# Performance work log

Hardware: AMD Instinct MI355X
Metric: run time of the kernel (lower is better)

## Reference

```python
import jax, jax.numpy as jnp
import numpy as np

DT = 0.05        # Euler step size
S_EULER = 2      # Euler steps between consecutive events, and after the last one (prop_to_end)


def setup_inputs() -> dict:
    key = jax.random.key(0)
    B, H, D, K, E = 512, 512, 128, 64, 256
    ks = jax.random.split(key, 16)

    def w(k, fan_in, fan_out):
        return jax.random.normal(k, (fan_in, fan_out), jnp.float32) / np.float32(np.sqrt(fan_in))

    X = jax.random.normal(ks[0], (K, E, D), jnp.float32)
    M = jax.random.bernoulli(ks[1], 0.5, (K, E, D)).astype(jnp.float32)
    # unique sample indices per event (irregular observation pattern, no scatter collisions)
    batch_idx = jax.vmap(lambda k: jax.random.permutation(k, B)[:E])(jax.random.split(ks[2], K))
    sample_idx = jnp.arange(B)
    b = lambda n: jnp.full((n,), 0.01, jnp.float32)  # torch init: bias filled with 0.01
    return {
        'X': X, 'M': M, 'batch_idx': batch_idx, 'sample_idx': sample_idx,
        'Wi': w(ks[3], D + H, H), 'bi': b(H),
        'Wf': w(ks[4], D + H, H), 'bf': b(H),
        'Wo': w(ks[5], D + H, H), 'bo': b(H),
        'Wc': w(ks[6], D + H, H), 'bc': b(H),
        'W1': w(ks[7], H, H), 'b1': b(H),
        'W2': w(ks[8], H, H), 'b2': b(H),
        'Wp1': w(ks[9], H, H), 'bp1': b(H),
        'Wp2': w(ks[10], H, D), 'bp2': b(D),
    }


def reference(X, M, batch_idx, sample_idx,
              Wi, bi, Wf, bf, Wo, bo, Wc, bc,
              W1, b1, W2, b2, Wp1, bp1, Wp2, bp2):
    B = sample_idx.shape[0]
    H = W1.shape[0]
    h0 = jnp.zeros((B, H), X.dtype)
    c0 = jnp.zeros((B, H), X.dtype)

    def euler(h):  # h <- h + dt * ODEFunc(h)
        return h + DT * (jnp.tanh(h @ W1 + b1) @ W2 + b2)

    def p_model(h):  # Linear -> ReLU -> (Dropout p=0, eval) -> Linear
        return jax.nn.relu(h @ Wp1 + bp1) @ Wp2 + bp2

    def step(carry, xs):
        h, c, loss, tot_m = carry
        Xo, Mo, idx = xs  # [E,D], [E,D], [E]
        for _ in range(S_EULER):
            h = euler(h)
        p = p_model(h)
        loss = loss + jnp.sum(jnp.abs(Xo - p[idx]) * Mo)
        tot_m = tot_m + jnp.sum(Mo)
        inp = jnp.concatenate([Xo, h[idx]], axis=-1)  # [E, D+H]
        ig = jax.nn.sigmoid(inp @ Wi + bi)
        fg = jax.nn.sigmoid(inp @ Wf + bf)
        og = jax.nn.sigmoid(inp @ Wo + bo)
        ct = jnp.tanh(inp @ Wc + bc)
        c_new = fg * c[idx] + ig * ct
        h_new = og * jnp.tanh(c_new)
        return (h.at[idx].set(h_new), c.at[idx].set(c_new), loss, tot_m), None

    init = (h0, c0, jnp.float32(0.0), jnp.float32(0.0))
    (h, c, loss, tot_m), _ = jax.lax.scan(step, init, (X, M, batch_idx))
    for _ in range(S_EULER):  # prop_to_end up to T
        h = euler(h)
    return jnp.stack([loss, loss / tot_m])
```

## Files before the change

kernel.cpp:

```cpp
#include <hip/hip_runtime.h>
#include <hip/hip_fp16.h>
#include <stdint.h>

#define Kn 64
#define En 256
#define Bn 512
#define Hn 512
#define Dn 128
#define NBLK 256
#define NTH  256
#define DT_C 0.05f


typedef _Float16 f16x8 __attribute__((ext_vector_type(8)));
typedef float    f32x4 __attribute__((ext_vector_type(4)));
typedef unsigned long long u64;

__device__ __forceinline__ float sigm(float x){ return 1.0f/(1.0f + __expf(-x)); }

__device__ __forceinline__ u64 ald(const u64* p){
  return __hip_atomic_load(p, __ATOMIC_RELAXED, __HIP_MEMORY_SCOPE_AGENT);
}
__device__ __forceinline__ void ast(u64* p, u64 v){
  __hip_atomic_store(p, v, __ATOMIC_RELAXED, __HIP_MEMORY_SCOPE_AGENT);
}

union HU { __half h[8]; u64 q[2]; };

__global__ void k_init(int* __restrict__ pos, float* __restrict__ acc,
                       int* __restrict__ flg, uint32_t* __restrict__ hf){
  int i = blockIdx.x*blockDim.x + threadIdx.x;
  if (i < Kn*Bn) pos[i] = -1;
  if (i < 2) acc[i] = 0.0f;
  if (i < 32*8*32) flg[i] = 0;
  if (i < Hn*Hn/2) hf[i] = 0;
}

__global__ void k_scatter(const int* __restrict__ bidx, int* __restrict__ pos){
  int i = blockIdx.x*blockDim.x + threadIdx.x;
  if (i < Kn*En){
    int k = i >> 8;
    int e = i & (En-1);
    pos[(k << 9) | bidx[i]] = e;
  }
}

__global__ void k_cvt_frag(const float* __restrict__ src, __half* __restrict__ dst,
                           int KT, int N, int n){
  int i = blockIdx.x*blockDim.x + threadIdx.x;
  if (i >= n) return;
  int C = i / (KT*512);
  int r = i % (KT*512);
  int T = r >> 9;
  int q = r & 511;
  int l = q >> 3, e = q & 7;
  int srow = T*32 + ((l>>4)<<3) + e;
  int scol = C*16 + (l&15);
  dst[i] = __float2half(src[(size_t)srow*N + scol]);
}

__device__ __forceinline__ f32x4 mv16(const __half* Af, const f16x8* Wr, int lane){
  f32x4 a = {0.f,0.f,0.f,0.f};
  #pragma unroll
  for (int kt=0; kt<16; kt++){
    f16x8 av = *(const f16x8*)(Af + kt*512 + lane*8);
    a = __builtin_amdgcn_mfma_f32_16x16x32_f16(av, Wr[kt], a, 0,0,0);
  }
  return a;
}

__global__ __launch_bounds__(NTH, 1) void k_main(
  const float* __restrict__ X, const float* __restrict__ Mm,
  const int* __restrict__ pos, const __half* __restrict__ WF,
  __half* __restrict__ Hf, __half* __restrict__ Tf,
  __half* __restrict__ T2f, __half* __restrict__ Hf2,
  const float* __restrict__ bi_, const float* __restrict__ bf_,
  const float* __restrict__ bo_, const float* __restrict__ bc_,
  const float* __restrict__ b1_, const float* __restrict__ b2_,
  const float* __restrict__ bp1_, const float* __restrict__ bp2_,
  float* __restrict__ acc, int* __restrict__ flg)
{
  const __half* W1F  = WF;
  const __half* W2F  = WF + 262144;
  const __half* Wp1F = WF + 524288;
  const __half* Wp2F = WF + 786432;
  const __half* WgF  = WF + 851968;

  const int t    = threadIdx.x;
  const int bid  = blockIdx.x;
  const int s    = bid & 7;
  const int g    = bid >> 3;
  const int w    = t >> 6;
  const int lane = t & 63;
  int* flgbase = flg + g*8*32;

  __shared__ __align__(16) __half Afrag[16*512];
  __shared__ __align__(16) __half Bfrag[16*512];
  __shared__ __align__(16) __half Xfrag[4*512];
  __shared__ __align__(16) float  outb[20*256];
  __shared__ float redbuf[8];

  const int row = t >> 4;
  const int q4  = t & 15;
  const int sc  = s*64 + q4*4;
  float Hreg[4] = {0,0,0,0};
  float Creg[4] = {0,0,0,0};
  float vb1[4], vb2[4], vbp1[4], vbi[4], vbf[4], vbo[4], vbc[4];
  #pragma unroll
  for (int i=0;i<4;i++){
    vb1[i]=b1_[sc+i]; vb2[i]=b2_[sc+i]; vbp1[i]=bp1_[sc+i];
    vbi[i]=bi_[sc+i]; vbf[i]=bf_[sc+i]; vbo[i]=bo_[sc+i]; vbc[i]=bc_[sc+i];
  }
  const float vbp2 = bp2_[s*16 + q4];

  f16x8 W1r[16], W2r[16], Wp1r[16];
  {
    const size_t cb = (size_t)(s*4 + w)*16*512 + (size_t)lane*8;
    #pragma unroll
    for (int kt=0; kt<16; kt++){
      W1r[kt]  = *(const f16x8*)(W1F  + cb + kt*512);
      W2r[kt]  = *(const f16x8*)(W2F  + cb + kt*512);
      Wp1r[kt] = *(const f16x8*)(Wp1F + cb + kt*512);
    }
  }

  float loss_loc = 0.f, m_loc = 0.f;
  int rnd = 0;
  const int grow = g*16 + row;

#define POLL() do{                                                         \
    if (t < 8){                                                            \
      while (__hip_atomic_load(flgbase + t*32, __ATOMIC_RELAXED,           \
                               __HIP_MEMORY_SCOPE_AGENT) < rnd)            \
        __builtin_amdgcn_s_sleep(1);                                       \
    }                                                                      \
    __syncthreads();                                                       \
  }while(0)

#define PUBLISH() do{                                                      \
    asm volatile("s_waitcnt vmcnt(0)" ::: "memory");                       \
    __syncthreads();                                                       \
    rnd++;                                                                 \
    if (t == 0)                                                            \
      __hip_atomic_store(flgbase + s*32, rnd, __ATOMIC_RELAXED,            \
                         __HIP_MEMORY_SCOPE_AGENT);                        \
  }while(0)

#define STAGE(DST, SRCPTR) do{                                             \
    const int ar = t & 15, ch = t >> 4;                                    \
    const u64* sp = (const u64*)((SRCPTR) + ((size_t)(g*16+ar))*512 + ch*32); \
    u64 v[8];                                                              \
    _Pragma("unroll") for (int i=0;i<8;i++) v[i] = ald(sp+i);              \
    _Pragma("unroll")                                                      \
    for (int kg=0;kg<4;kg++){                                              \
      u64* d = (u64*)((DST) + ch*512 + (ar + 16*kg)*8);                    \
      d[0] = v[2*kg]; d[1] = v[2*kg+1];                                    \
    }                                                                      \
  }while(0)

  for (int k=0; k<Kn; k++){
    const int epos = pos[(k<<9) + grow];

    POLL();
    if (k > 0) STAGE(Bfrag, T2f);
    {
      const int ar = t & 15, ch = t >> 4;
      const __half* hsrc = Hf;
      if (k > 0 && pos[((k-1)<<9) + g*16 + ar] >= 0) hsrc = Hf2;
      const u64* sp = (const u64*)(hsrc + ((size_t)(g*16+ar))*512 + ch*32);
      u64 v[8];
      #pragma unroll
      for (int i=0;i<8;i++) v[i] = ald(sp+i);
      #pragma unroll
      for (int kg=0;kg<4;kg++){
        u64* d = (u64*)(Afrag + ch*512 + (ar + 16*kg)*8);
        d[0] = v[2*kg]; d[1] = v[2*kg+1];
      }
    }
    __syncthreads();
    {
      f32x4 a4 = mv16(Afrag, W1r, lane);
      float* o = outb + w*256 + ((lane>>4)*4)*16 + (lane&15);
      o[0]=a4[0]; o[16]=a4[1]; o[32]=a4[2]; o[48]=a4[3];
    }
    if (k > 0){
      const __half* wb = Wp2F + (size_t)s*16*512;
      f32x4 a4 = {0,0,0,0};
      #pragma unroll
      for (int kt2=0; kt2<4; kt2++){
        const int kt = w*4 + kt2;
        f16x8 a = *(const f16x8*)(Bfrag + kt*512 + lane*8);
        f16x8 b = *(const f16x8*)(wb + kt*512 + lane*8);
        a4 = __builtin_amdgcn_mfma_f32_16x16x32_f16(a, b, a4, 0,0,0);
      }
      float* o = outb + (16+w)*256 + ((lane>>4)*4)*16 + (lane&15);
      o[0]=a4[0]; o[16]=a4[1]; o[32]=a4[2]; o[48]=a4[3];
    }
    __syncthreads();
    {
      const float* o = outb + (q4>>2)*256 + row*16 + (q4&3)*4;
      HU u;
      u.h[0]=__float2half(tanhf(o[0]+vb1[0])); u.h[1]=__float2half(tanhf(o[1]+vb1[1]));
      u.h[2]=__float2half(tanhf(o[2]+vb1[2])); u.h[3]=__float2half(tanhf(o[3]+vb1[3]));
      ast((u64*)(Tf + (size_t)grow*512 + sc), u.q[0]);
    }
    PUBLISH();
    if (k > 0){
      const int ep = pos[((k-1)<<9) + g*16 + row];
      if (ep >= 0){
        float p = outb[16*256 + row*16+q4] + outb[17*256 + row*16+q4]
                + outb[18*256 + row*16+q4] + outb[19*256 + row*16+q4] + vbp2;
        const size_t xo = ((size_t)((k-1)*En+ep))*Dn + s*16 + q4;
        float mo = Mm[xo];
        loss_loc += fabsf(X[xo] - p)*mo;
        m_loc    += mo;
      }
    }

    POLL();
    STAGE(Afrag, Tf);
    __syncthreads();
    {
      f32x4 a4 = mv16(Afrag, W2r, lane);
      float* o = outb + w*256 + ((lane>>4)*4)*16 + (lane&15);
      o[0]=a4[0]; o[16]=a4[1]; o[32]=a4[2]; o[48]=a4[3];
    }
    __syncthreads();
    {
      const float* o = outb + (q4>>2)*256 + row*16 + (q4&3)*4;
      HU u;
      Hreg[0] += DT_C*(o[0]+vb2[0]); Hreg[1] += DT_C*(o[1]+vb2[1]);
      Hreg[2] += DT_C*(o[2]+vb2[2]); Hreg[3] += DT_C*(o[3]+vb2[3]);
      u.h[0]=__float2half(Hreg[0]); u.h[1]=__float2half(Hreg[1]);
      u.h[2]=__float2half(Hreg[2]); u.h[3]=__float2half(Hreg[3]);
      ast((u64*)(Hf + (size_t)grow*512 + sc), u.q[0]);
    }
    PUBLISH();

    POLL();
    STAGE(Afrag, Hf);
    __syncthreads();
    {
      f32x4 a4 = mv16(Afrag, W1r, lane);
      float* o = outb + w*256 + ((lane>>4)*4)*16 + (lane&15);
      o[0]=a4[0]; o[16]=a4[1]; o[32]=a4[2]; o[48]=a4[3];
    }
    __syncthreads();
    {
      const float* o = outb + (q4>>2)*256 + row*16 + (q4&3)*4;
      HU u;
      u.h[0]=__float2half(tanhf(o[0]+vb1[0])); u.h[1]=__float2half(tanhf(o[1]+vb1[1]));
      u.h[2]=__float2half(tanhf(o[2]+vb1[2])); u.h[3]=__float2half(tanhf(o[3]+vb1[3]));
      ast((u64*)(Tf + (size_t)grow*512 + sc), u.q[0]);
    }
    PUBLISH();

    POLL();
    STAGE(Afrag, Tf);
    __syncthreads();
    {
      f32x4 a4 = mv16(Afrag, W2r, lane);
      float* o = outb + w*256 + ((lane>>4)*4)*16 + (lane&15);
      o[0]=a4[0]; o[16]=a4[1]; o[32]=a4[2]; o[48]=a4[3];
    }
    __syncthreads();
    {
      const float* o = outb + (q4>>2)*256 + row*16 + (q4&3)*4;
      HU u;
      Hreg[0] += DT_C*(o[0]+vb2[0]); Hreg[1] += DT_C*(o[1]+vb2[1]);
      Hreg[2] += DT_C*(o[2]+vb2[2]); Hreg[3] += DT_C*(o[3]+vb2[3]);
      u.h[0]=__float2half(Hreg[0]); u.h[1]=__float2half(Hreg[1]);
      u.h[2]=__float2half(Hreg[2]); u.h[3]=__float2half(Hreg[3]);
      ast((u64*)(Hf + (size_t)grow*512 + sc), u.q[0]);
    }
    PUBLISH();

    POLL();
    STAGE(Afrag, Hf);
    if (t < 64){
      const int ar = t & 15, ch = t >> 4;
      const int e = pos[(k<<9) + g*16 + ar];
      float xv[32];
      if (e >= 0){
        const float4* xp = (const float4*)(X + ((size_t)(k*En+e))*Dn + ch*32);
        #pragma unroll
        for (int i=0;i<8;i++){
          float4 f = xp[i];
          xv[4*i]=f.x; xv[4*i+1]=f.y; xv[4*i+2]=f.z; xv[4*i+3]=f.w;
        }
      } else {
        #pragma unroll
        for (int i=0;i<32;i++) xv[i]=0.f;
      }
      #pragma unroll
      for (int kg=0;kg<4;kg++){
        HU u;
        #pragma unroll
        for (int e8=0;e8<8;e8++) u.h[e8] = __float2half(xv[kg*8+e8]);
        u64* d = (u64*)(Xfrag + ch*512 + (ar + 16*kg)*8);
        d[0] = u.q[0]; d[1] = u.q[1];
      }
    }
    __syncthreads();
    {
      f32x4 a4 = mv16(Afrag, Wp1r, lane);
      float* o = outb + (16+w)*256 + ((lane>>4)*4)*16 + (lane&15);
      o[0]=a4[0]; o[16]=a4[1]; o[32]=a4[2]; o[48]=a4[3];
    }
    #pragma unroll 1
    for (int i=0;i<4;i++){
      const int Cg = w*32 + s*4 + i;
      const __half* wb = WgF + (size_t)Cg*20*512;
      f32x4 a4 = {0,0,0,0};
      #pragma unroll 4
      for (int kt=0; kt<4; kt++){
        f16x8 a = *(const f16x8*)(Xfrag + kt*512 + lane*8);
        f16x8 b = *(const f16x8*)(wb + kt*512 + lane*8);
        a4 = __builtin_amdgcn_mfma_f32_16x16x32_f16(a, b, a4, 0,0,0);
      }
      #pragma unroll 4
      for (int kt=4; kt<20; kt++){
        f16x8 a = *(const f16x8*)(Afrag + (kt-4)*512 + lane*8);
        f16x8 b = *(const f16x8*)(wb + kt*512 + lane*8);
        a4 = __builtin_amdgcn_mfma_f32_16x16x32_f16(a, b, a4, 0,0,0);
      }
      float* o = outb + (w*4+i)*256 + ((lane>>4)*4)*16 + (lane&15);
      o[0]=a4[0]; o[16]=a4[1]; o[32]=a4[2]; o[48]=a4[3];
    }
    __syncthreads();
    {
      const float* o = outb + (16+(q4>>2))*256 + row*16 + (q4&3)*4;
      HU u;
      u.h[0]=__float2half(fmaxf(o[0]+vbp1[0],0.f));
      u.h[1]=__float2half(fmaxf(o[1]+vbp1[1],0.f));
      u.h[2]=__float2half(fmaxf(o[2]+vbp1[2],0.f));
      u.h[3]=__float2half(fmaxf(o[3]+vbp1[3],0.f));
      ast((u64*)(T2f + (size_t)grow*512 + sc), u.q[0]);
    }
    if (epos >= 0){
      const int sub = q4 >> 2, off = row*16 + (q4&3)*4;
      const float4 pi = *(const float4*)(outb + (0*4+sub)*256 + off);
      const float4 pf = *(const float4*)(outb + (1*4+sub)*256 + off);
      const float4 po = *(const float4*)(outb + (2*4+sub)*256 + off);
      const float4 pc = *(const float4*)(outb + (3*4+sub)*256 + off);
      HU hu;
      const float gi[4]={pi.x,pi.y,pi.z,pi.w}, gf[4]={pf.x,pf.y,pf.z,pf.w};
      const float go[4]={po.x,po.y,po.z,po.w}, gc[4]={pc.x,pc.y,pc.z,pc.w};
      #pragma unroll
      for (int i=0;i<4;i++){
        float ig = sigm(gi[i] + vbi[i]);
        float fg = sigm(gf[i] + vbf[i]);
        float og = sigm(go[i] + vbo[i]);
        float ct = tanhf(gc[i] + vbc[i]);
        Creg[i] = fg*Creg[i] + ig*ct;
        Hreg[i] = og*tanhf(Creg[i]);
        hu.h[i] = __float2half(Hreg[i]);
      }
      ast((u64*)(Hf2 + (size_t)grow*512 + sc), hu.q[0]);
    }
    PUBLISH();
  }

  POLL();
  STAGE(Bfrag, T2f);
  __syncthreads();
  {
    const __half* wb = Wp2F + (size_t)s*16*512;
    f32x4 a4 = {0,0,0,0};
    #pragma unroll
    for (int kt2=0; kt2<4; kt2++){
      const int kt = w*4 + kt2;
      f16x8 a = *(const f16x8*)(Bfrag + kt*512 + lane*8);
      f16x8 b = *(const f16x8*)(wb + kt*512 + lane*8);
      a4 = __builtin_amdgcn_mfma_f32_16x16x32_f16(a, b, a4, 0,0,0);
    }
    float* o = outb + (16+w)*256 + ((lane>>4)*4)*16 + (lane&15);
    o[0]=a4[0]; o[16]=a4[1]; o[32]=a4[2]; o[48]=a4[3];
  }
  __syncthreads();
  {
    const int ep = pos[((Kn-1)<<9) + g*16 + row];
    if (ep >= 0){
      float p = outb[16*256 + row*16+q4] + outb[17*256 + row*16+q4]
              + outb[18*256 + row*16+q4] + outb[19*256 + row*16+q4] + vbp2;
      const size_t xo = ((size_t)((Kn-1)*En+ep))*Dn + s*16 + q4;
      float mo = Mm[xo];
      loss_loc += fabsf(X[xo] - p)*mo;
      m_loc    += mo;
    }
  }

  #pragma unroll
  for (int off=32; off>0; off>>=1){
    loss_loc += __shfl_down(loss_loc, off);
    m_loc    += __shfl_down(m_loc, off);
  }
  if (lane == 0){ redbuf[w] = loss_loc; redbuf[4+w] = m_loc; }
  __syncthreads();
  if (t == 0){
    atomicAdd(acc+0, redbuf[0]+redbuf[1]+redbuf[2]+redbuf[3]);
    atomicAdd(acc+1, redbuf[4]+redbuf[5]+redbuf[6]+redbuf[7]);
  }
#undef POLL
#undef PUBLISH
#undef STAGE
}

__global__ void k_fin(const float* __restrict__ acc, float* __restrict__ out){
  if (threadIdx.x == 0){
    out[0] = acc[0];
    out[1] = acc[0]/acc[1];
  }
}

extern "C" void kernel_launch(void* const* d_in, const int* in_sizes, int n_in,
                              void* d_out, int out_size, void* d_ws, size_t ws_size,
                              hipStream_t stream)
{
  const float* X   = (const float*)d_in[0];
  const float* Mm  = (const float*)d_in[1];
  const int*  bidx = (const int*)d_in[2];
  const float* Wi  = (const float*)d_in[4];
  const float* bi  = (const float*)d_in[5];
  const float* Wf  = (const float*)d_in[6];
  const float* bff = (const float*)d_in[7];
  const float* Wo  = (const float*)d_in[8];
  const float* bo  = (const float*)d_in[9];
  const float* Wc  = (const float*)d_in[10];
  const float* bc  = (const float*)d_in[11];
  const float* W1  = (const float*)d_in[12];
  const float* b1  = (const float*)d_in[13];
  const float* W2  = (const float*)d_in[14];
  const float* b2  = (const float*)d_in[15];
  const float* Wp1 = (const float*)d_in[16];
  const float* bp1 = (const float*)d_in[17];
  const float* Wp2 = (const float*)d_in[18];
  const float* bp2 = (const float*)d_in[19];

  char* ws = (char*)d_ws;
  int*    pos = (int*)ws;
  float*  acc = (float*)(ws + 131072);
  int*    flg = (int*)(ws + 196608);
  __half* Hf  = (__half*)(ws + 1048576);
  __half* Tf  = (__half*)(ws + 1572864);
  __half* T2f = (__half*)(ws + 2097152);
  __half* Hf2 = (__half*)(ws + 2621440);
  __half* WF  = (__half*)(ws + 4194304);

  k_init   <<<512, 256, 0, stream>>>(pos, acc, flg, (uint32_t*)Hf);
  k_scatter<<<(Kn*En + 255)/256, 256, 0, stream>>>(bidx, pos);

  k_cvt_frag<<<(262144+255)/256, 256, 0, stream>>>(W1,  WF,          16, 512, 262144);
  k_cvt_frag<<<(262144+255)/256, 256, 0, stream>>>(W2,  WF + 262144, 16, 512, 262144);
  k_cvt_frag<<<(262144+255)/256, 256, 0, stream>>>(Wp1, WF + 524288, 16, 512, 262144);
  k_cvt_frag<<<(65536 +255)/256, 256, 0, stream>>>(Wp2, WF + 786432, 16, 128, 65536);
  k_cvt_frag<<<(327680+255)/256, 256, 0, stream>>>(Wi,  WF + 851968,            20, 512, 327680);
  k_cvt_frag<<<(327680+255)/256, 256, 0, stream>>>(Wf,  WF + 851968 + 327680,   20, 512, 327680);
  k_cvt_frag<<<(327680+255)/256, 256, 0, stream>>>(Wo,  WF + 851968 + 655360,   20, 512, 327680);
  k_cvt_frag<<<(327680+255)/256, 256, 0, stream>>>(Wc,  WF + 851968 + 983040,   20, 512, 327680);

  k_main<<<NBLK, NTH, 0, stream>>>(X, Mm, pos, WF, Hf, Tf, T2f, Hf2,
                                   bi, bff, bo, bc, b1, b2, bp1, bp2, acc, flg);
  k_fin<<<1, 64, 0, stream>>>(acc, (float*)d_out);
}
```

Baseline: 1.893 ms.

## Halve block count so each block handles two row groups interleaved

Drops the persistent grid from 256 to 128 blocks. Each block now processes two 16-row groups in turn within every phase, keeping separate H/C register state per group and polling or publishing per-group flags. While one group waits on its flags, the other group's work can fill the gap, and fewer blocks share the MI355X's CUs. The cost is twice the serial work per block on the critical path, which may lengthen each phase.

```diff
diff --git a/kernel.cpp b/kernel.cpp
--- a/kernel.cpp
+++ b/kernel.cpp
@@ -7,7 +7,7 @@
 #define Bn 512
 #define Hn 512
 #define Dn 128
-#define NBLK 256
+#define NBLK 128
 #define NTH  256
 #define DT_C 0.05f
 
@@ -89,10 +89,9 @@
   const int t    = threadIdx.x;
   const int bid  = blockIdx.x;
   const int s    = bid & 7;
-  const int g    = bid >> 3;
+  const int qp   = bid >> 3;
   const int w    = t >> 6;
   const int lane = t & 63;
-  int* flgbase = flg + g*8*32;
 
   __shared__ __align__(16) __half Afrag[16*512];
   __shared__ __align__(16) __half Bfrag[16*512];
@@ -103,8 +102,8 @@
   const int row = t >> 4;
   const int q4  = t & 15;
   const int sc  = s*64 + q4*4;
-  float Hreg[4] = {0,0,0,0};
-  float Creg[4] = {0,0,0,0};
+  float Hreg[2][4] = {{0,0,0,0},{0,0,0,0}};
+  float Creg[2][4] = {{0,0,0,0},{0,0,0,0}};
   float vb1[4], vb2[4], vbp1[4], vbi[4], vbf[4], vbo[4], vbc[4];
   #pragma unroll
   for (int i=0;i<4;i++){
@@ -126,29 +125,27 @@
 
   float loss_loc = 0.f, m_loc = 0.f;
   int rnd = 0;
-  const int grow = g*16 + row;
-
-#define POLL() do{                                                         \
+
+#define POLLF(FB, R) do{                                                   \
     if (t < 8){                                                            \
-      while (__hip_atomic_load(flgbase + t*32, __ATOMIC_RELAXED,           \
-                               __HIP_MEMORY_SCOPE_AGENT) < rnd)            \
+      while (__hip_atomic_load((FB) + t*32, __ATOMIC_RELAXED,              \
+                               __HIP_MEMORY_SCOPE_AGENT) < (R))            \
         __builtin_amdgcn_s_sleep(1);                                       \
     }                                                                      \
     __syncthreads();                                                       \
   }while(0)
 
-#define PUBLISH() do{                                                      \
+#define PUBF(FB, R) do{                                                    \
     asm volatile("s_waitcnt vmcnt(0)" ::: "memory");                       \
     __syncthreads();                                                       \
-    rnd++;                                                                 \
     if (t == 0)                                                            \
-      __hip_atomic_store(flgbase + s*32, rnd, __ATOMIC_RELAXED,            \
+      __hip_atomic_store((FB) + s*32, (R), __ATOMIC_RELAXED,               \
                          __HIP_MEMORY_SCOPE_AGENT);                        \
   }while(0)
 
-#define STAGE(DST, SRCPTR) do{                                             \
+#define STAGE(DST, SRCPTR, G) do{                                          \
     const int ar = t & 15, ch = t >> 4;                                    \
-    const u64* sp = (const u64*)((SRCPTR) + ((size_t)(g*16+ar))*512 + ch*32); \
+    const u64* sp = (const u64*)((SRCPTR) + ((size_t)((G)*16+ar))*512 + ch*32); \
     u64 v[8];                                                              \
     _Pragma("unroll") for (int i=0;i<8;i++) v[i] = ald(sp+i);              \
     _Pragma("unroll")                                                      \
@@ -159,31 +156,250 @@
   }while(0)
 
   for (int k=0; k<Kn; k++){
-    const int epos = pos[(k<<9) + grow];
-
-    POLL();
-    if (k > 0) STAGE(Bfrag, T2f);
-    {
-      const int ar = t & 15, ch = t >> 4;
-      const __half* hsrc = Hf;
-      if (k > 0 && pos[((k-1)<<9) + g*16 + ar] >= 0) hsrc = Hf2;
-      const u64* sp = (const u64*)(hsrc + ((size_t)(g*16+ar))*512 + ch*32);
-      u64 v[8];
-      #pragma unroll
-      for (int i=0;i<8;i++) v[i] = ald(sp+i);
-      #pragma unroll
-      for (int kg=0;kg<4;kg++){
-        u64* d = (u64*)(Afrag + ch*512 + (ar + 16*kg)*8);
-        d[0] = v[2*kg]; d[1] = v[2*kg+1];
-      }
-    }
+    #pragma unroll
+    for (int c=0;c<2;c++){
+      const int g = qp*2 + c;
+      int* fb = flg + g*8*32;
+      const int grow = g*16 + row;
+      POLLF(fb, rnd);
+      if (k > 0) STAGE(Bfrag, T2f, g);
+      {
+        const int ar = t & 15, ch = t >> 4;
+        const __half* hsrc = Hf;
+        if (k > 0 && pos[((k-1)<<9) + g*16 + ar] >= 0) hsrc = Hf2;
+        const u64* sp = (const u64*)(hsrc + ((size_t)(g*16+ar))*512 + ch*32);
+        u64 v[8];
+        #pragma unroll
+        for (int i=0;i<8;i++) v[i] = ald(sp+i);
+        #pragma unroll
+        for (int kg=0;kg<4;kg++){
+          u64* d = (u64*)(Afrag + ch*512 + (ar + 16*kg)*8);
+          d[0] = v[2*kg]; d[1] = v[2*kg+1];
+        }
+      }
+      __syncthreads();
+      {
+        f32x4 a4 = mv16(Afrag, W1r, lane);
+        float* o = outb + w*256 + ((lane>>4)*4)*16 + (lane&15);
+        o[0]=a4[0]; o[16]=a4[1]; o[32]=a4[2]; o[48]=a4[3];
+      }
+      if (k > 0){
+        const __half* wb = Wp2F + (size_t)s*16*512;
+        f32x4 a4 = {0,0,0,0};
+        #pragma unroll
+        for (int kt2=0; kt2<4; kt2++){
+          const int kt = w*4 + kt2;
+          f16x8 a = *(const f16x8*)(Bfrag + kt*512 + lane*8);
+          f16x8 b = *(const f16x8*)(wb + kt*512 + lane*8);
+          a4 = __builtin_amdgcn_mfma_f32_16x16x32_f16(a, b, a4, 0,0,0);
+        }
+        float* o = outb + (16+w)*256 + ((lane>>4)*4)*16 + (lane&15);
+        o[0]=a4[0]; o[16]=a4[1]; o[32]=a4[2]; o[48]=a4[3];
+      }
+      __syncthreads();
+      {
+        const float* o = outb + (q4>>2)*256 + row*16 + (q4&3)*4;
+        HU u;
+        u.h[0]=__float2half(tanhf(o[0]+vb1[0])); u.h[1]=__float2half(tanhf(o[1]+vb1[1]));
+        u.h[2]=__float2half(tanhf(o[2]+vb1[2])); u.h[3]=__float2half(tanhf(o[3]+vb1[3]));
+        ast((u64*)(Tf + (size_t)grow*512 + sc), u.q[0]);
+      }
+      PUBF(fb, rnd+1);
+      if (k > 0){
+        const int ep = pos[((k-1)<<9) + g*16 + row];
+        if (ep >= 0){
+          float p = outb[16*256 + row*16+q4] + outb[17*256 + row*16+q4]
+                  + outb[18*256 + row*16+q4] + outb[19*256 + row*16+q4] + vbp2;
+          const size_t xo = ((size_t)((k-1)*En+ep))*Dn + s*16 + q4;
+          float mo = Mm[xo];
+          loss_loc += fabsf(X[xo] - p)*mo;
+          m_loc    += mo;
+        }
+      }
+    }
+    rnd++;
+
+    #pragma unroll
+    for (int c=0;c<2;c++){
+      const int g = qp*2 + c;
+      int* fb = flg + g*8*32;
+      const int grow = g*16 + row;
+      POLLF(fb, rnd);
+      STAGE(Afrag, Tf, g);
+      __syncthreads();
+      {
+        f32x4 a4 = mv16(Afrag, W2r, lane);
+        float* o = outb + w*256 + ((lane>>4)*4)*16 + (lane&15);
+        o[0]=a4[0]; o[16]=a4[1]; o[32]=a4[2]; o[48]=a4[3];
+      }
+      __syncthreads();
+      {
+        const float* o = outb + (q4>>2)*256 + row*16 + (q4&3)*4;
+        HU u;
+        Hreg[c][0] += DT_C*(o[0]+vb2[0]); Hreg[c][1] += DT_C*(o[1]+vb2[1]);
+        Hreg[c][2] += DT_C*(o[2]+vb2[2]); Hreg[c][3] += DT_C*(o[3]+vb2[3]);
+        u.h[0]=__float2half(Hreg[c][0]); u.h[1]=__float2half(Hreg[c][1]);
+        u.h[2]=__float2half(Hreg[c][2]); u.h[3]=__float2half(Hreg[c][3]);
+        ast((u64*)(Hf + (size_t)grow*512 + sc), u.q[0]);
+      }
+      PUBF(fb, rnd+1);
+    }
+    rnd++;
+
+    #pragma unroll
+    for (int c=0;c<2;c++){
+      const int g = qp*2 + c;
+      int* fb = flg + g*8*32;
+      const int grow = g*16 + row;
+      POLLF(fb, rnd);
+      STAGE(Afrag, Hf, g);
+      __syncthreads();
+      {
+        f32x4 a4 = mv16(Afrag, W1r, lane);
+        float* o = outb + w*256 + ((lane>>4)*4)*16 + (lane&15);
+        o[0]=a4[0]; o[16]=a4[1]; o[32]=a4[2]; o[48]=a4[3];
+      }
+      __syncthreads();
+      {
+        const float* o = outb + (q4>>2)*256 + row*16 + (q4&3)*4;
+        HU u;
+        u.h[0]=__float2half(tanhf(o[0]+vb1[0])); u.h[1]=__float2half(tanhf(o[1]+vb1[1]));
+        u.h[2]=__float2half(tanhf(o[2]+vb1[2])); u.h[3]=__float2half(tanhf(o[3]+vb1[3]));
+        ast((u64*)(Tf + (size_t)grow*512 + sc), u.q[0]);
+      }
+      PUBF(fb, rnd+1);
+    }
+    rnd++;
+
+    #pragma unroll
+    for (int c=0;c<2;c++){
+      const int g = qp*2 + c;
+      int* fb = flg + g*8*32;
+      const int grow = g*16 + row;
+      POLLF(fb, rnd);
+      STAGE(Afrag, Tf, g);
+      __syncthreads();
+      {
+        f32x4 a4 = mv16(Afrag, W2r, lane);
+        float* o = outb + w*256 + ((lane>>4)*4)*16 + (lane&15);
+        o[0]=a4[0]; o[16]=a4[1]; o[32]=a4[2]; o[48]=a4[3];
+      }
+      __syncthreads();
+      {
+        const float* o = outb + (q4>>2)*256 + row*16 + (q4&3)*4;
+        HU u;
+        Hreg[c][0] += DT_C*(o[0]+vb2[0]); Hreg[c][1] += DT_C*(o[1]+vb2[1]);
+        Hreg[c][2] += DT_C*(o[2]+vb2[2]); Hreg[c][3] += DT_C*(o[3]+vb2[3]);
+        u.h[0]=__float2half(Hreg[c][0]); u.h[1]=__float2half(Hreg[c][1]);
+        u.h[2]=__float2half(Hreg[c][2]); u.h[3]=__float2half(Hreg[c][3]);
+        ast((u64*)(Hf + (size_t)grow*512 + sc), u.q[0]);
+      }
+      PUBF(fb, rnd+1);
+    }
+    rnd++;
+
+    #pragma unroll
+    for (int c=0;c<2;c++){
+      const int g = qp*2 + c;
+      int* fb = flg + g*8*32;
+      const int grow = g*16 + row;
+      const int epos = pos[(k<<9) + grow];
+      POLLF(fb, rnd);
+      STAGE(Afrag, Hf, g);
+      if (t < 64){
+        const int ar = t & 15, ch = t >> 4;
+        const int e = pos[(k<<9) + g*16 + ar];
+        float xv[32];
+        if (e >= 0){
+          const float4* xp = (const float4*)(X + ((size_t)(k*En+e))*Dn + ch*32);
+          #pragma unroll
+          for (int i=0;i<8;i++){
+            float4 f = xp[i];
+            xv[4*i]=f.x; xv[4*i+1]=f.y; xv[4*i+2]=f.z; xv[4*i+3]=f.w;
+          }
+        } else {
+          #pragma unroll
+          for (int i=0;i<32;i++) xv[i]=0.f;
+        }
+        #pragma unroll
+        for (int kg=0;kg<4;kg++){
+          HU u;
+          #pragma unroll
+          for (int e8=0;e8<8;e8++) u.h[e8] = __float2half(xv[kg*8+e8]);
+          u64* d = (u64*)(Xfrag + ch*512 + (ar + 16*kg)*8);
+          d[0] = u.q[0]; d[1] = u.q[1];
+        }
+      }
+      __syncthreads();
+      {
+        f32x4 a4 = mv16(Afrag, Wp1r, lane);
+        float* o = outb + (16+w)*256 + ((lane>>4)*4)*16 + (lane&15);
+        o[0]=a4[0]; o[16]=a4[1]; o[32]=a4[2]; o[48]=a4[3];
+      }
+      #pragma unroll 1
+      for (int i=0;i<4;i++){
+        const int Cg = w*32 + s*4 + i;
+        const __half* wb = WgF + (size_t)Cg*20*512;
+        f32x4 a4 = {0,0,0,0};
+        #pragma unroll 4
+        for (int kt=0; kt<4; kt++){
+          f16x8 a = *(const f16x8*)(Xfrag + kt*512 + lane*8);
+          f16x8 b = *(const f16x8*)(wb + kt*512 + lane*8);
+          a4 = __builtin_amdgcn_mfma_f32_16x16x32_f16(a, b, a4, 0,0,0);
+        }
+        #pragma unroll 4
+        for (int kt=4; kt<20; kt++){
+          f16x8 a = *(const f16x8*)(Afrag + (kt-4)*512 + lane*8);
+          f16x8 b = *(const f16x8*)(wb + kt*512 + lane*8);
+          a4 = __builtin_amdgcn_mfma_f32_16x16x32_f16(a, b, a4, 0,0,0);
+        }
+        float* o = outb + (w*4+i)*256 + ((lane>>4)*4)*16 + (lane&15);
+        o[0]=a4[0]; o[16]=a4[1]; o[32]=a4[2]; o[48]=a4[3];
+      }
+      __syncthreads();
+      {
+        const float* o = outb + (16+(q4>>2))*256 + row*16 + (q4&3)*4;
+        HU u;
+        u.h[0]=__float2half(fmaxf(o[0]+vbp1[0],0.f));
+        u.h[1]=__float2half(fmaxf(o[1]+vbp1[1],0.f));
+        u.h[2]=__float2half(fmaxf(o[2]+vbp1[2],0.f));
+        u.h[3]=__float2half(fmaxf(o[3]+vbp1[3],0.f));
+        ast((u64*)(T2f + (size_t)grow*512 + sc), u.q[0]);
+      }
+      if (epos >= 0){
+        const int sub = q4 >> 2, off = row*16 + (q4&3)*4;
+        const float4 pi = *(const float4*)(outb + (0*4+sub)*256 + off);
+        const float4 pf = *(const float4*)(outb + (1*4+sub)*256 + off);
+        const float4 po = *(const float4*)(outb + (2*4+sub)*256 + off);
+        const float4 pc = *(const float4*)(outb + (3*4+sub)*256 + off);
+        HU hu;
+        const float gi[4]={pi.x,pi.y,pi.z,pi.w}, gf[4]={pf.x,pf.y,pf.z,pf.w};
+        const float go[4]={po.x,po.y,po.z,po.w}, gc[4]={pc.x,pc.y,pc.z,pc.w};
+        #pragma unroll
+        for (int i=0;i<4;i++){
+          float ig = sigm(gi[i] + vbi[i]);
+          float fg = sigm(gf[i] + vbf[i]);
+          float og = sigm(go[i] + vbo[i]);
+          float ct = tanhf(gc[i] + vbc[i]);
+          Creg[c][i] = fg*Creg[c][i] + ig*ct;
+          Hreg[c][i] = og*tanhf(Creg[c][i]);
+          hu.h[i] = __float2half(Hreg[c][i]);
+        }
+        ast((u64*)(Hf2 + (size_t)grow*512 + sc), hu.q[0]);
+      }
+      PUBF(fb, rnd+1);
+    }
+    rnd++;
+  }
+
+  #pragma unroll
+  for (int c=0;c<2;c++){
+    const int g = qp*2 + c;
+    int* fb = flg + g*8*32;
+    POLLF(fb, rnd);
+    STAGE(Bfrag, T2f, g);
     __syncthreads();
     {
-      f32x4 a4 = mv16(Afrag, W1r, lane);
-      float* o = outb + w*256 + ((lane>>4)*4)*16 + (lane&15);
-      o[0]=a4[0]; o[16]=a4[1]; o[32]=a4[2]; o[48]=a4[3];
-    }
-    if (k > 0){
       const __half* wb = Wp2F + (size_t)s*16*512;
       f32x4 a4 = {0,0,0,0};
       #pragma unroll
@@ -198,196 +414,17 @@
     }
     __syncthreads();
     {
-      const float* o = outb + (q4>>2)*256 + row*16 + (q4&3)*4;
-      HU u;
-      u.h[0]=__float2half(tanhf(o[0]+vb1[0])); u.h[1]=__float2half(tanhf(o[1]+vb1[1]));
-      u.h[2]=__float2half(tanhf(o[2]+vb1[2])); u.h[3]=__float2half(tanhf(o[3]+vb1[3]));
-      ast((u64*)(Tf + (size_t)grow*512 + sc), u.q[0]);
-    }
-    PUBLISH();
-    if (k > 0){
-      const int ep = pos[((k-1)<<9) + g*16 + row];
+      const int ep = pos[((Kn-1)<<9) + g*16 + row];
       if (ep >= 0){
         float p = outb[16*256 + row*16+q4] + outb[17*256 + row*16+q4]
                 + outb[18*256 + row*16+q4] + outb[19*256 + row*16+q4] + vbp2;
-        const size_t xo = ((size_t)((k-1)*En+ep))*Dn + s*16 + q4;
+        const size_t xo = ((size_t)((Kn-1)*En+ep))*Dn + s*16 + q4;
         float mo = Mm[xo];
         loss_loc += fabsf(X[xo] - p)*mo;
         m_loc    += mo;
       }
     }
-
-    POLL();
-    STAGE(Afrag, Tf);
     __syncthreads();
-    {
-      f32x4 a4 = mv16(Afrag, W2r, lane);
-      float* o = outb + w*256 + ((lane>>4)*4)*16 + (lane&15);
-      o[0]=a4[0]; o[16]=a4[1]; o[32]=a4[2]; o[48]=a4[3];
-    }
-    __syncthreads();
-    {
-      const float* o = outb + (q4>>2)*256 + row*16 + (q4&3)*4;
-      HU u;
-      Hreg[0] += DT_C*(o[0]+vb2[0]); Hreg[1] += DT_C*(o[1]+vb2[1]);
-      Hreg[2] += DT_C*(o[2]+vb2[2]); Hreg[3] += DT_C*(o[3]+vb2[3]);
-      u.h[0]=__float2half(Hreg[0]); u.h[1]=__float2half(Hreg[1]);
-      u.h[2]=__float2half(Hreg[2]); u.h[3]=__float2half(Hreg[3]);
-      ast((u64*)(Hf + (size_t)grow*512 + sc), u.q[0]);
-    }
-    PUBLISH();
-
-    POLL();
-    STAGE(Afrag, Hf);
-    __syncthreads();
-    {
-      f32x4 a4 = mv16(Afrag, W1r, lane);
-      float* o = outb + w*256 + ((lane>>4)*4)*16 + (lane&15);
-      o[0]=a4[0]; o[16]=a4[1]; o[32]=a4[2]; o[48]=a4[3];
-    }
-    __syncthreads();
-    {
-      const float* o = outb + (q4>>2)*256 + row*16 + (q4&3)*4;
-      HU u;
-      u.h[0]=__float2half(tanhf(o[0]+vb1[0])); u.h[1]=__float2half(tanhf(o[1]+vb1[1]));
-      u.h[2]=__float2half(tanhf(o[2]+vb1[2])); u.h[3]=__float2half(tanhf(o[3]+vb1[3]));
-      ast((u64*)(Tf + (size_t)grow*512 + sc), u.q[0]);
-    }
-    PUBLISH();
-
-    POLL();
-    STAGE(Afrag, Tf);
-    __syncthreads();
-    {
-      f32x4 a4 = mv16(Afrag, W2r, lane);
-      float* o = outb + w*256 + ((lane>>4)*4)*16 + (lane&15);
-      o[0]=a4[0]; o[16]=a4[1]; o[32]=a4[2]; o[48]=a4[3];
-    }
-    __syncthreads();
-    {
-      const float* o = outb + (q4>>2)*256 + row*16 + (q4&3)*4;
-      HU u;
-      Hreg[0] += DT_C*(o[0]+vb2[0]); Hreg[1] += DT_C*(o[1]+vb2[1]);
-      Hreg[2] += DT_C*(o[2]+vb2[2]); Hreg[3] += DT_C*(o[3]+vb2[3]);
-      u.h[0]=__float2half(Hreg[0]); u.h[1]=__float2half(Hreg[1]);
-      u.h[2]=__float2half(Hreg[2]); u.h[3]=__float2half(Hreg[3]);
-      ast((u64*)(Hf + (size_t)grow*512 + sc), u.q[0]);
-    }
-    PUBLISH();
-
-    POLL();
-    STAGE(Afrag, Hf);
-    if (t < 64){
-      const int ar = t & 15, ch = t >> 4;
-      const int e = pos[(k<<9) + g*16 + ar];
-      float xv[32];
-      if (e >= 0){
-        const float4* xp = (const float4*)(X + ((size_t)(k*En+e))*Dn + ch*32);
-        #pragma unroll
-        for (int i=0;i<8;i++){
-          float4 f = xp[i];
-          xv[4*i]=f.x; xv[4*i+1]=f.y; xv[4*i+2]=f.z; xv[4*i+3]=f.w;
-        }
-      } else {
-        #pragma unroll
-        for (int i=0;i<32;i++) xv[i]=0.f;
-      }
-      #pragma unroll
-      for (int kg=0;kg<4;kg++){
-        HU u;
-        #pragma unroll
-        for (int e8=0;e8<8;e8++) u.h[e8] = __float2half(xv[kg*8+e8]);
-        u64* d = (u64*)(Xfrag + ch*512 + (ar + 16*kg)*8);
-        d[0] = u.q[0]; d[1] = u.q[1];
-      }
-    }
-    __syncthreads();
-    {
-      f32x4 a4 = mv16(Afrag, Wp1r, lane);
-      float* o = outb + (16+w)*256 + ((lane>>4)*4)*16 + (lane&15);
-      o[0]=a4[0]; o[16]=a4[1]; o[32]=a4[2]; o[48]=a4[3];
-    }
-    #pragma unroll 1
-    for (int i=0;i<4;i++){
-      const int Cg = w*32 + s*4 + i;
-      const __half* wb = WgF + (size_t)Cg*20*512;
-      f32x4 a4 = {0,0,0,0};
-      #pragma unroll 4
-      for (int kt=0; kt<4; kt++){
-        f16x8 a = *(const f16x8*)(Xfrag + kt*512 + lane*8);
-        f16x8 b = *(const f16x8*)(wb + kt*512 + lane*8);
-        a4 = __builtin_amdgcn_mfma_f32_16x16x32_f16(a, b, a4, 0,0,0);
-      }
-      #pragma unroll 4
-      for (int kt=4; kt<20; kt++){
-        f16x8 a = *(const f16x8*)(Afrag + (kt-4)*512 + lane*8);
-        f16x8 b = *(const f16x8*)(wb + kt*512 + lane*8);
-        a4 = __builtin_amdgcn_mfma_f32_16x16x32_f16(a, b, a4, 0,0,0);
-      }
-      float* o = outb + (w*4+i)*256 + ((lane>>4)*4)*16 + (lane&15);
-      o[0]=a4[0]; o[16]=a4[1]; o[32]=a4[2]; o[48]=a4[3];
-    }
-    __syncthreads();
-    {
-      const float* o = outb + (16+(q4>>2))*256 + row*16 + (q4&3)*4;
-      HU u;
-      u.h[0]=__float2half(fmaxf(o[0]+vbp1[0],0.f));
-      u.h[1]=__float2half(fmaxf(o[1]+vbp1[1],0.f));
-      u.h[2]=__float2half(fmaxf(o[2]+vbp1[2],0.f));
-      u.h[3]=__float2half(fmaxf(o[3]+vbp1[3],0.f));
-      ast((u64*)(T2f + (size_t)grow*512 + sc), u.q[0]);
-    }
-    if (epos >= 0){
-      const int sub = q4 >> 2, off = row*16 + (q4&3)*4;
-      const float4 pi = *(const float4*)(outb + (0*4+sub)*256 + off);
-      const float4 pf = *(const float4*)(outb + (1*4+sub)*256 + off);
-      const float4 po = *(const float4*)(outb + (2*4+sub)*256 + off);
-      const float4 pc = *(const float4*)(outb + (3*4+sub)*256 + off);
-      HU hu;
-      const float gi[4]={pi.x,pi.y,pi.z,pi.w}, gf[4]={pf.x,pf.y,pf.z,pf.w};
-      const float go[4]={po.x,po.y,po.z,po.w}, gc[4]={pc.x,pc.y,pc.z,pc.w};
-      #pragma unroll
-      for (int i=0;i<4;i++){
-        float ig = sigm(gi[i] + vbi[i]);
-        float fg = sigm(gf[i] + vbf[i]);
-        float og = sigm(go[i] + vbo[i]);
-        float ct = tanhf(gc[i] + vbc[i]);
-        Creg[i] = fg*Creg[i] + ig*ct;
-        Hreg[i] = og*tanhf(Creg[i]);
-        hu.h[i] = __float2half(Hreg[i]);
-      }
-      ast((u64*)(Hf2 + (size_t)grow*512 + sc), hu.q[0]);
-    }
-    PUBLISH();
-  }
-
-  POLL();
-  STAGE(Bfrag, T2f);
-  __syncthreads();
-  {
-    const __half* wb = Wp2F + (size_t)s*16*512;
-    f32x4 a4 = {0,0,0,0};
-    #pragma unroll
-    for (int kt2=0; kt2<4; kt2++){
-      const int kt = w*4 + kt2;
-      f16x8 a = *(const f16x8*)(Bfrag + kt*512 + lane*8);
-      f16x8 b = *(const f16x8*)(wb + kt*512 + lane*8);
-      a4 = __builtin_amdgcn_mfma_f32_16x16x32_f16(a, b, a4, 0,0,0);
-    }
-    float* o = outb + (16+w)*256 + ((lane>>4)*4)*16 + (lane&15);
-    o[0]=a4[0]; o[16]=a4[1]; o[32]=a4[2]; o[48]=a4[3];
-  }
-  __syncthreads();
-  {
-    const int ep = pos[((Kn-1)<<9) + g*16 + row];
-    if (ep >= 0){
-      float p = outb[16*256 + row*16+q4] + outb[17*256 + row*16+q4]
-              + outb[18*256 + row*16+q4] + outb[19*256 + row*16+q4] + vbp2;
-      const size_t xo = ((size_t)((Kn-1)*En+ep))*Dn + s*16 + q4;
-      float mo = Mm[xo];
-      loss_loc += fabsf(X[xo] - p)*mo;
-      m_loc    += mo;
-    }
   }
 
   #pragma unroll
@@ -401,8 +438,8 @@
     atomicAdd(acc+0, redbuf[0]+redbuf[1]+redbuf[2]+redbuf[3]);
     atomicAdd(acc+1, redbuf[4]+redbuf[5]+redbuf[6]+redbuf[7]);
   }
-#undef POLL
-#undef PUBLISH
+#undef POLLF
+#undef PUBF
 #undef STAGE
 }
 
```

Result: slower. 3.463 ms (+83.0%).

## Use XCD-local L2 loads and stores for cross-block exchange when groups share an XCD

Applied to the files above, without the earlier changes.

At startup each block records its XCC_ID, and each group of 8 cooperating blocks decides whether all members sit on the same XCD and the placement is not uniform. If so, the flag polling and the fragment loads use sc0 loads that skip L1 but stay in the local L2, and the stores are plain volatile ones, instead of agent-scope atomics. This aims to cut the latency of the many per-round handshakes. Groups that do not qualify, and polls that spin too long, fall back to the atomic path. The risk is correctness: it relies on the XCD mapping and on cache coherence behaviour of non-atomic accesses, and the startup handshake adds a little latency.

```diff
diff --git a/kernel.cpp b/kernel.cpp
--- a/kernel.cpp
+++ b/kernel.cpp
@@ -24,16 +24,52 @@
 __device__ __forceinline__ void ast(u64* p, u64 v){
   __hip_atomic_store(p, v, __ATOMIC_RELAXED, __HIP_MEMORY_SCOPE_AGENT);
 }
+__device__ __forceinline__ int ai_ld(const int* p){
+  return __hip_atomic_load(p, __ATOMIC_RELAXED, __HIP_MEMORY_SCOPE_AGENT);
+}
+__device__ __forceinline__ void ai_st(int* p, int v){
+  __hip_atomic_store(p, v, __ATOMIC_RELAXED, __HIP_MEMORY_SCOPE_AGENT);
+}
+
+__device__ __forceinline__ void ld8(const u64* p, u64 v[8], int fast){
+  if (fast){
+    asm volatile(
+      "global_load_dwordx2 %0, %8, off sc0\n\t"
+      "global_load_dwordx2 %1, %8, off offset:8 sc0\n\t"
+      "global_load_dwordx2 %2, %8, off offset:16 sc0\n\t"
+      "global_load_dwordx2 %3, %8, off offset:24 sc0\n\t"
+      "global_load_dwordx2 %4, %8, off offset:32 sc0\n\t"
+      "global_load_dwordx2 %5, %8, off offset:40 sc0\n\t"
+      "global_load_dwordx2 %6, %8, off offset:48 sc0\n\t"
+      "global_load_dwordx2 %7, %8, off offset:56 sc0\n\t"
+      "s_waitcnt vmcnt(0)"
+      : "=&v"(v[0]),"=&v"(v[1]),"=&v"(v[2]),"=&v"(v[3]),
+        "=&v"(v[4]),"=&v"(v[5]),"=&v"(v[6]),"=&v"(v[7])
+      : "v"(p) : "memory");
+  } else {
+    #pragma unroll
+    for (int i=0;i<8;i++) v[i] = ald(p+i);
+  }
+}
+__device__ __forceinline__ void st1(u64* p, u64 v, int fast){
+  if (fast) *(volatile u64*)p = v;
+  else      ast(p, v);
+}
 
 union HU { __half h[8]; u64 q[2]; };
 
 __global__ void k_init(int* __restrict__ pos, float* __restrict__ acc,
-                       int* __restrict__ flg, uint32_t* __restrict__ hf){
+                       int* __restrict__ flg, uint32_t* __restrict__ hf,
+                       int* __restrict__ xcdrec, int* __restrict__ xsane,
+                       int* __restrict__ xdec){
   int i = blockIdx.x*blockDim.x + threadIdx.x;
   if (i < Kn*Bn) pos[i] = -1;
   if (i < 2) acc[i] = 0.0f;
   if (i < 32*8*32) flg[i] = 0;
   if (i < Hn*Hn/2) hf[i] = 0;
+  if (i < 256) xcdrec[i] = 0;
+  if (i < 1) xsane[0] = 0;
+  if (i < 32*32) xdec[i] = 0;
 }
 
 __global__ void k_scatter(const int* __restrict__ bidx, int* __restrict__ pos){
@@ -78,7 +114,8 @@
   const float* __restrict__ bo_, const float* __restrict__ bc_,
   const float* __restrict__ b1_, const float* __restrict__ b2_,
   const float* __restrict__ bp1_, const float* __restrict__ bp2_,
-  float* __restrict__ acc, int* __restrict__ flg)
+  float* __restrict__ acc, int* __restrict__ flg,
+  int* __restrict__ xcdrec, int* __restrict__ xsane, int* __restrict__ xdec)
 {
   const __half* W1F  = WF;
   const __half* W2F  = WF + 262144;
@@ -99,6 +136,54 @@
   __shared__ __align__(16) __half Xfrag[4*512];
   __shared__ __align__(16) float  outb[20*256];
   __shared__ float redbuf[8];
+  __shared__ int   xsh[8];
+  __shared__ int   decsh;
+
+  int fastD, fastF;
+  {
+    int myxcd;
+    asm volatile("s_getreg_b32 %0, hwreg(HW_REG_XCC_ID)" : "=s"(myxcd));
+    if (t == 0) ai_st(xcdrec + bid, myxcd + 1);
+    if (bid == 0){
+      int v;
+      while ((v = ai_ld(xcdrec + t)) == 0) __builtin_amdgcn_s_sleep(1);
+      ((int*)outb)[t] = v;
+      __syncthreads();
+      if (t == 0){
+        int mn = ((int*)outb)[0], mx = mn;
+        for (int i=1;i<256;i++){
+          int u = ((int*)outb)[i];
+          mn = u < mn ? u : mn; mx = u > mx ? u : mx;
+        }
+        ai_st(xsane, (mn != mx) ? 1 : 2);
+      }
+      __syncthreads();
+    }
+    if (s == 0){
+      if (t < 8){
+        int v;
+        while ((v = ai_ld(xcdrec + g*8 + t)) == 0) __builtin_amdgcn_s_sleep(1);
+        xsh[t] = v;
+      }
+      __syncthreads();
+      if (t == 0){
+        int sane;
+        while ((sane = ai_ld(xsane)) == 0) __builtin_amdgcn_s_sleep(1);
+        bool eq = true;
+        #pragma unroll
+        for (int i=1;i<8;i++) eq = eq && (xsh[i] == xsh[0]);
+        ai_st(xdec + g*32, (eq && sane == 1) ? 1 : 2);
+      }
+    }
+    if (t == 0){
+      int d;
+      while ((d = ai_ld(xdec + g*32)) == 0) __builtin_amdgcn_s_sleep(1);
+      decsh = d;
+    }
+    __syncthreads();
+    fastD = (decsh == 1);
+    fastF = fastD;
+  }
 
   const int row = t >> 4;
   const int q4  = t & 15;
@@ -128,34 +213,52 @@
   int rnd = 0;
   const int grow = g*16 + row;
 
-#define POLL() do{                                                         \
-    if (t < 8){                                                            \
-      while (__hip_atomic_load(flgbase + t*32, __ATOMIC_RELAXED,           \
-                               __HIP_MEMORY_SCOPE_AGENT) < rnd)            \
-        __builtin_amdgcn_s_sleep(1);                                       \
-    }                                                                      \
-    __syncthreads();                                                       \
+#define POLL() do{                                                          \
+    if (w == 0){                                                            \
+      bool okk = true;                                                      \
+      if (lane < 8){                                                        \
+        const int* fp = flgbase + lane*32;                                  \
+        if (fastF){                                                         \
+          int spn = 0;                                                      \
+          while (1){                                                        \
+            int v;                                                          \
+            asm volatile("global_load_dword %0, %1, off sc0\n\t"            \
+                         "s_waitcnt vmcnt(0)"                               \
+                         : "=&v"(v) : "v"(fp) : "memory");                  \
+            if (v >= rnd) break;                                            \
+            if (++spn > 2048){ okk = false; break; }                        \
+            __builtin_amdgcn_s_sleep(1);                                    \
+          }                                                                 \
+        }                                                                   \
+        if (!fastF || !okk){                                                \
+          while (ai_ld(fp) < rnd) __builtin_amdgcn_s_sleep(1);              \
+        }                                                                   \
+      }                                                                     \
+      if (__any(!okk)) fastF = 0;                                           \
+    }                                                                       \
+    __syncthreads();                                                        \
   }while(0)
 
-#define PUBLISH() do{                                                      \
-    asm volatile("s_waitcnt vmcnt(0)" ::: "memory");                       \
-    __syncthreads();                                                       \
-    rnd++;                                                                 \
-    if (t == 0)                                                            \
-      __hip_atomic_store(flgbase + s*32, rnd, __ATOMIC_RELAXED,            \
-                         __HIP_MEMORY_SCOPE_AGENT);                        \
+#define PUBLISH() do{                                                       \
+    asm volatile("s_waitcnt vmcnt(0)" ::: "memory");                        \
+    __syncthreads();                                                        \
+    rnd++;                                                                  \
+    if (t == 0){                                                            \
+      if (fastD) *(volatile int*)(flgbase + s*32) = rnd;                    \
+      ai_st(flgbase + s*32, rnd);                                           \
+    }                                                                       \
   }while(0)
 
-#define STAGE(DST, SRCPTR) do{                                             \
-    const int ar = t & 15, ch = t >> 4;                                    \
+#define STAGE(DST, SRCPTR) do{                                              \
+    const int ar = t & 15, ch = t >> 4;                                     \
     const u64* sp = (const u64*)((SRCPTR) + ((size_t)(g*16+ar))*512 + ch*32); \
-    u64 v[8];                                                              \
-    _Pragma("unroll") for (int i=0;i<8;i++) v[i] = ald(sp+i);              \
-    _Pragma("unroll")                                                      \
-    for (int kg=0;kg<4;kg++){                                              \
-      u64* d = (u64*)((DST) + ch*512 + (ar + 16*kg)*8);                    \
-      d[0] = v[2*kg]; d[1] = v[2*kg+1];                                    \
-    }                                                                      \
+    u64 v[8];                                                               \
+    ld8(sp, v, fastD);                                                      \
+    _Pragma("unroll")                                                       \
+    for (int kg=0;kg<4;kg++){                                               \
+      u64* d = (u64*)((DST) + ch*512 + (ar + 16*kg)*8);                     \
+      d[0] = v[2*kg]; d[1] = v[2*kg+1];                                     \
+    }                                                                       \
   }while(0)
 
   for (int k=0; k<Kn; k++){
@@ -169,8 +272,7 @@
       if (k > 0 && pos[((k-1)<<9) + g*16 + ar] >= 0) hsrc = Hf2;
       const u64* sp = (const u64*)(hsrc + ((size_t)(g*16+ar))*512 + ch*32);
       u64 v[8];
-      #pragma unroll
-      for (int i=0;i<8;i++) v[i] = ald(sp+i);
+      ld8(sp, v, fastD);
       #pragma unroll
       for (int kg=0;kg<4;kg++){
         u64* d = (u64*)(Afrag + ch*512 + (ar + 16*kg)*8);
@@ -202,7 +304,7 @@
       HU u;
       u.h[0]=__float2half(tanhf(o[0]+vb1[0])); u.h[1]=__float2half(tanhf(o[1]+vb1[1]));
       u.h[2]=__float2half(tanhf(o[2]+vb1[2])); u.h[3]=__float2half(tanhf(o[3]+vb1[3]));
-      ast((u64*)(Tf + (size_t)grow*512 + sc), u.q[0]);
+      st1((u64*)(Tf + (size_t)grow*512 + sc), u.q[0], fastD);
     }
     PUBLISH();
     if (k > 0){
@@ -233,7 +335,7 @@
       Hreg[2] += DT_C*(o[2]+vb2[2]); Hreg[3] += DT_C*(o[3]+vb2[3]);
       u.h[0]=__float2half(Hreg[0]); u.h[1]=__float2half(Hreg[1]);
       u.h[2]=__float2half(Hreg[2]); u.h[3]=__float2half(Hreg[3]);
-      ast((u64*)(Hf + (size_t)grow*512 + sc), u.q[0]);
+      st1((u64*)(Hf + (size_t)grow*512 + sc), u.q[0], fastD);
     }
     PUBLISH();
 
@@ -251,7 +353,7 @@
       HU u;
       u.h[0]=__float2half(tanhf(o[0]+vb1[0])); u.h[1]=__float2half(tanhf(o[1]+vb1[1]));
       u.h[2]=__float2half(tanhf(o[2]+vb1[2])); u.h[3]=__float2half(tanhf(o[3]+vb1[3]));
-      ast((u64*)(Tf + (size_t)grow*512 + sc), u.q[0]);
+      st1((u64*)(Tf + (size_t)grow*512 + sc), u.q[0], fastD);
     }
     PUBLISH();
 
@@ -271,7 +373,7 @@
       Hreg[2] += DT_C*(o[2]+vb2[2]); Hreg[3] += DT_C*(o[3]+vb2[3]);
       u.h[0]=__float2half(Hreg[0]); u.h[1]=__float2half(Hreg[1]);
       u.h[2]=__float2half(Hreg[2]); u.h[3]=__float2half(Hreg[3]);
-      ast((u64*)(Hf + (size_t)grow*512 + sc), u.q[0]);
+      st1((u64*)(Hf + (size_t)grow*512 + sc), u.q[0], fastD);
     }
     PUBLISH();
 
@@ -335,7 +437,7 @@
       u.h[1]=__float2half(fmaxf(o[1]+vbp1[1],0.f));
       u.h[2]=__float2half(fmaxf(o[2]+vbp1[2],0.f));
       u.h[3]=__float2half(fmaxf(o[3]+vbp1[3],0.f));
-      ast((u64*)(T2f + (size_t)grow*512 + sc), u.q[0]);
+      st1((u64*)(T2f + (size_t)grow*512 + sc), u.q[0], fastD);
     }
     if (epos >= 0){
       const int sub = q4 >> 2, off = row*16 + (q4&3)*4;
@@ -356,7 +458,7 @@
         Hreg[i] = og*tanhf(Creg[i]);
         hu.h[i] = __float2half(Hreg[i]);
       }
-      ast((u64*)(Hf2 + (size_t)grow*512 + sc), hu.q[0]);
+      st1((u64*)(Hf2 + (size_t)grow*512 + sc), hu.q[0], fastD);
     }
     PUBLISH();
   }
@@ -438,16 +540,19 @@
   const float* bp2 = (const float*)d_in[19];
 
   char* ws = (char*)d_ws;
-  int*    pos = (int*)ws;
-  float*  acc = (float*)(ws + 131072);
-  int*    flg = (int*)(ws + 196608);
-  __half* Hf  = (__half*)(ws + 1048576);
-  __half* Tf  = (__half*)(ws + 1572864);
-  __half* T2f = (__half*)(ws + 2097152);
-  __half* Hf2 = (__half*)(ws + 2621440);
-  __half* WF  = (__half*)(ws + 4194304);
-
-  k_init   <<<512, 256, 0, stream>>>(pos, acc, flg, (uint32_t*)Hf);
+  int*    pos  = (int*)ws;
+  float*  acc  = (float*)(ws + 131072);
+  int*    xrec = (int*)(ws + 163840);
+  int*    xsan = (int*)(ws + 164864);
+  int*    xdec = (int*)(ws + 165888);
+  int*    flg  = (int*)(ws + 196608);
+  __half* Hf   = (__half*)(ws + 1048576);
+  __half* Tf   = (__half*)(ws + 1572864);
+  __half* T2f  = (__half*)(ws + 2097152);
+  __half* Hf2  = (__half*)(ws + 2621440);
+  __half* WF   = (__half*)(ws + 4194304);
+
+  k_init   <<<512, 256, 0, stream>>>(pos, acc, flg, (uint32_t*)Hf, xrec, xsan, xdec);
   k_scatter<<<(Kn*En + 255)/256, 256, 0, stream>>>(bidx, pos);
 
   k_cvt_frag<<<(262144+255)/256, 256, 0, stream>>>(W1,  WF,          16, 512, 262144);
@@ -460,6 +565,7 @@
   k_cvt_frag<<<(327680+255)/256, 256, 0, stream>>>(Wc,  WF + 851968 + 983040,   20, 512, 327680);
 
   k_main<<<NBLK, NTH, 0, stream>>>(X, Mm, pos, WF, Hf, Tf, T2f, Hf2,
-                                   bi, bff, bo, bc, b1, b2, bp1, bp2, acc, flg);
+                                   bi, bff, bo, bc, b1, b2, bp1, bp2, acc, flg,
+                                   xrec, xsan, xdec);
   k_fin<<<1, 64, 0, stream>>>(acc, (float*)d_out);
 }
```

After: 1.921 ms. No clear change (+1.5%).
